# Kernel tuning notes

Hardware: AMD Instinct MI355X
Metric: run time of the kernel (lower is better)

## Reference

```python
import jax, jax.numpy as jnp
from jax import lax
import numpy as np

D_MODEL = 512
MODES = 16
B, S = 8, 4096
EPS = 1e-5


def setup_inputs() -> dict:
    key = jax.random.key(0)
    ks = jax.random.split(key, 7)
    x = jax.random.normal(ks[0], (B, S, D_MODEL), dtype=jnp.float32)
    gamma = jnp.ones((D_MODEL,), dtype=jnp.float32)
    beta = jnp.zeros((D_MODEL,), dtype=jnp.float32)
    # complex spectral weights stored as real/imag parts, torch init: randn(cfloat)*0.02
    wr = jax.random.normal(ks[1], (D_MODEL, MODES), dtype=jnp.float32) * 0.02
    wi = jax.random.normal(ks[2], (D_MODEL, MODES), dtype=jnp.float32) * 0.02
    # Conv1d(d_model, d_model, 3): weight (out, in, k), torch default uniform(-b, b)
    bound = 1.0 / np.sqrt(D_MODEL * 3)
    conv_w = jax.random.uniform(ks[3], (D_MODEL, D_MODEL, 3), dtype=jnp.float32, minval=-bound, maxval=bound)
    conv_b = jax.random.uniform(ks[4], (D_MODEL,), dtype=jnp.float32, minval=-bound, maxval=bound)
    return {"x": x, "gamma": gamma, "beta": beta, "wr": wr, "wi": wi,
            "conv_w": conv_w, "conv_b": conv_b}


def reference(x, gamma, beta, wr, wi, conv_w, conv_b):
    Bq, Sq, Dq = x.shape
    residual = x
    # LayerNorm over last dim (biased variance, eps=1e-5)
    mu = jnp.mean(x, axis=-1, keepdims=True)
    var = jnp.var(x, axis=-1, keepdims=True)
    xn = (x - mu) * lax.rsqrt(var + EPS) * gamma + beta
    # truncated-mode spectral conv: rfft along seq, multiply first `modes` bins, irfft
    xf = jnp.fft.rfft(xn, axis=1, norm='ortho')           # [B, S//2+1, D] complex
    m = min(wr.shape[1], xf.shape[1])
    w = (wr + 1j * wi).T[:m]                              # [m, D]
    out_ft = jnp.zeros_like(xf).at[:, :m, :].set(xf[:, :m, :] * w[None])
    xs = jnp.fft.irfft(out_ft, n=Sq, axis=1, norm='ortho')  # [B, S, D] real
    # Conv1d(k=3, pad=1) over seq dim on channel-first layout
    xc = lax.conv_general_dilated(
        xs.transpose(0, 2, 1), conv_w, window_strides=(1,), padding=[(1, 1)],
        dimension_numbers=('NCH', 'OIH', 'NCH'))
    xc = (xc + conv_b[None, :, None]).transpose(0, 2, 1)
    return residual + xs + xc
```

## Files before the change

kernel.cpp:

```cpp
#include <hip/hip_runtime.h>
#include <hip/hip_bf16.h>
#include <math.h>

#define Bn 8
#define Sn 4096
#define Dn 512
#define MODES 16
#define ANGF 0.0015339807878856412f

#define PART_OFF 0
#define Y_OFF 8388608
#define WTF_OFF 8519680
#define ZP_OFF 9306112
#define G_OFF 10878976
#define V_OFF 11010048
#define STATS_OFF 11018240

__global__ __launch_bounds__(256) void k_transpose_w(
    const float* __restrict__ cw, float* __restrict__ wTf) {
  int idx = blockIdx.x * 256 + threadIdx.x;
  int o = idx & 511;
  int d = (idx >> 9) & 511;
  int t = idx >> 18;
  wTf[idx] = cw[o * 1536 + d * 3 + t];
}

__global__ __launch_bounds__(256) void k_stats(const float* __restrict__ x,
                                               float2* __restrict__ stats) {
  int wave = threadIdx.x >> 6, lane = threadIdx.x & 63;
  int row0 = blockIdx.x * 32 + wave * 8;
  for (int j = 0; j < 8; ++j) {
    int row = row0 + j;
    const float4* px = (const float4*)(x + ((size_t)row << 9));
    float4 v0 = px[lane * 2];
    float4 v1 = px[lane * 2 + 1];
    float ps = v0.x + v0.y + v0.z + v0.w + v1.x + v1.y + v1.z + v1.w;
    float pq = v0.x * v0.x + v0.y * v0.y + v0.z * v0.z + v0.w * v0.w +
               v1.x * v1.x + v1.y * v1.y + v1.z * v1.z + v1.w * v1.w;
#pragma unroll
    for (int off = 32; off > 0; off >>= 1) {
      ps += __shfl_down(ps, off);
      pq += __shfl_down(pq, off);
    }
    if (lane == 0) {
      float mu = ps * (1.0f / Dn);
      float var = pq * (1.0f / Dn) - mu * mu;
      stats[row] = make_float2(mu, rsqrtf(var + 1e-5f));
    }
  }
}

__global__ __launch_bounds__(256) void k_project(
    const float* __restrict__ x, const float* __restrict__ gamma,
    const float* __restrict__ beta, const float2* __restrict__ stats,
    float* __restrict__ partials) {
  int blk = blockIdx.x;
  int b = blk >> 7;
  int c = (blk >> 1) & 63;
  int dh = blk & 1;
  int tid = threadIdx.x;
  int s_base = c * 64;
  int d = dh * 256 + tid;

  __shared__ float2 s_tw[64 * MODES];
  __shared__ float2 s_mv[64];
  if (tid < 64) s_mv[tid] = stats[(b << 12) + s_base + tid];
#pragma unroll
  for (int u = 0; u < 4; u++) {
    int e = tid * 4 + u;
    int r = e >> 4, k = e & 15;
    int m = ((s_base + r) * k) & (Sn - 1);
    float sn, cn;
    __sincosf((float)m * ANGF, &sn, &cn);
    s_tw[e] = make_float2(cn, sn);
  }
  __syncthreads();

  float g = gamma[d], be = beta[d];
  float accRe[MODES], accIm[MODES];
#pragma unroll
  for (int k = 0; k < MODES; k++) { accRe[k] = 0.f; accIm[k] = 0.f; }

  const float* xp = x + (((size_t)(b * Sn + s_base)) << 9) + d;
  float xv_n = xp[0];
  for (int r = 0; r < 64; ++r) {
    float xv = xv_n;
    if (r < 63) xv_n = xp[(size_t)(r + 1) << 9];
    float2 mv = s_mv[r];
    float xn = (xv - mv.x) * mv.y * g + be;
    const float2* tw = &s_tw[r * MODES];
#pragma unroll
    for (int k = 0; k < MODES; k++) {
      float2 cs = tw[k];
      accRe[k] += xn * cs.x;
      accIm[k] -= xn * cs.y;
    }
  }
  size_t base = ((size_t)(b * 64 + c)) * MODES;
  float2* P = (float2*)partials;
#pragma unroll
  for (int k = 0; k < MODES; k++)
    P[(base + k) * Dn + d] = make_float2(accRe[k], accIm[k]);
}

__global__ __launch_bounds__(256) void k_reduce_modes(
    const float* __restrict__ partials, const float* __restrict__ wr,
    const float* __restrict__ wi, float* __restrict__ Y) {
  int idx = blockIdx.x * 256 + threadIdx.x;
  int d = idx & 511;
  int k = (idx >> 9) & 15;
  int b = idx >> 13;
  const float2* P = (const float2*)partials;
  float re = 0.f, im = 0.f;
#pragma unroll 8
  for (int c = 0; c < 64; c++) {
    float2 p = P[(((size_t)(b * 64 + c)) * MODES + k) * Dn + d];
    re += p.x;
    im += p.y;
  }
  float wrv = wr[d * MODES + k];
  float wiv = wi[d * MODES + k];
  float yre = re * wrv - im * wiv;
  float yim = re * wiv + im * wrv;
  float scale = (k == 0) ? (1.0f / 4096.0f) : (2.0f / 4096.0f);
  ((float2*)Y)[((size_t)b * MODES + k) * Dn + d] =
      make_float2(yre * scale, yim * scale);
}

__global__ __launch_bounds__(256) void k_build_z(
    const float* __restrict__ Y, const float* __restrict__ wTf,
    float* __restrict__ Zp) {
  int blk = blockIdx.x;
  int b = blk / 96;
  int rem = blk % 96;
  int t = rem >> 5;
  int r2 = rem & 31;
  int och = r2 >> 2;
  int dch = r2 & 3;
  int tid = threadIdx.x;
  int oi = tid & 63, kq = tid >> 6;
  int o = och * 64 + oi;
  int d0 = dch * 128;

  __shared__ float2 Ys[MODES][128];
  const float2* Y2 = (const float2*)Y;
#pragma unroll
  for (int i = 0; i < 8; i++) {
    int e = tid + i * 256;
    int k = e >> 7, dd = e & 127;
    Ys[k][dd] = Y2[(((size_t)(b * MODES + k)) << 9) + d0 + dd];
  }
  __syncthreads();

  float zc[4] = {0.f, 0.f, 0.f, 0.f}, zs[4] = {0.f, 0.f, 0.f, 0.f};
  const float* wp = wTf + (((size_t)(t * Dn + d0)) << 9) + o;
  float wv_n = wp[0];
  for (int dd = 0; dd < 128; ++dd) {
    float wv = wv_n;
    if (dd < 127) wv_n = wp[(size_t)(dd + 1) << 9];
#pragma unroll
    for (int m = 0; m < 4; m++) {
      float2 y = Ys[kq * 4 + m][dd];
      zc[m] += y.x * wv;
      zs[m] += y.y * wv;
    }
  }
  float2* Z2 = (float2*)Zp;
#pragma unroll
  for (int m = 0; m < 4; m++) {
    int k = kq * 4 + m;
    Z2[(((size_t)(dch * 24 + b * 3 + t) * MODES + k)) << 9 | o] =
        make_float2(zc[m], zs[m]);
  }
}

__global__ __launch_bounds__(256) void k_build_g(
    const float* __restrict__ Y, const float* __restrict__ Zp,
    float* __restrict__ G, float* __restrict__ V) {
  int idx = blockIdx.x * 256 + threadIdx.x;
  const float2* Y2 = (const float2*)Y;
  const float2* Z2 = (const float2*)Zp;
  if (idx < 65536) {
    int o = idx & 511;
    int k = (idx >> 9) & 15;
    int b = idx >> 13;
    float2 z0 = make_float2(0.f, 0.f), z1 = z0, z2 = z0;
#pragma unroll
    for (int dch = 0; dch < 4; dch++) {
      float2 a0 = Z2[(((size_t)(dch * 24 + b * 3 + 0) * MODES + k)) << 9 | o];
      float2 a1 = Z2[(((size_t)(dch * 24 + b * 3 + 1) * MODES + k)) << 9 | o];
      float2 a2 = Z2[(((size_t)(dch * 24 + b * 3 + 2) * MODES + k)) << 9 | o];
      z0.x += a0.x; z0.y += a0.y;
      z1.x += a1.x; z1.y += a1.y;
      z2.x += a2.x; z2.y += a2.y;
    }
    float2 y = Y2[(((size_t)(b * MODES + k)) << 9) + o];
    float sf, cf;
    __sincosf((float)k * ANGF, &sf, &cf);
    float gc = y.x + (cf * z0.x + sf * z0.y) + z1.x + (cf * z2.x - sf * z2.y);
    float gs = y.y + (cf * z0.y - sf * z0.x) + z1.y + (cf * z2.y + sf * z2.x);
    G[(((size_t)(b * MODES + k) * 2 + 0)) << 9 | o] = gc;
    G[(((size_t)(b * MODES + k) * 2 + 1)) << 9 | o] = gs;
  } else if (idx < 65536 + 8192) {
    int j = idx - 65536;
    int o = j & 511;
    int comp = (j >> 9) & 1;
    int b = j >> 10;
    float v = 0.f;
#pragma unroll
    for (int k = 0; k < MODES; k++) {
      float2 z = make_float2(0.f, 0.f);
#pragma unroll
      for (int dch = 0; dch < 4; dch++) {
        float2 a = Z2[(((size_t)(dch * 24 + b * 3 + (comp ? 2 : 0)) * MODES +
                        k)) << 9 | o];
        z.x += a.x; z.y += a.y;
      }
      if (comp == 0) {
        float sf, cf;
        __sincosf((float)k * ANGF, &sf, &cf);
        v += cf * z.x + sf * z.y;
      } else {
        v += z.x;
      }
    }
    V[((size_t)(b * 2 + comp) << 9) + o] = v;
  }
}

__global__ __launch_bounds__(256) void k_apply(
    const float* __restrict__ x, const float* __restrict__ G,
    const float* __restrict__ V, const float* __restrict__ conv_b,
    float* __restrict__ out) {
  int b = blockIdx.x >> 7;
  int st = blockIdx.x & 127;
  int s0 = st * 32;
  int tid = threadIdx.x;
  int o0 = tid * 2;

  __shared__ float2 s_tw[32][MODES];
#pragma unroll
  for (int u = 0; u < 2; u++) {
    int e = tid * 2 + u;
    int r = e >> 4, k = e & 15;
    int m = ((s0 + r) * k) & (Sn - 1);
    float sn, cn;
    __sincosf((float)m * ANGF, &sn, &cn);
    s_tw[r][k] = make_float2(cn, sn);
  }

  float2 Gc[MODES], Gs[MODES];
  const float2* Gp = (const float2*)(G + ((size_t)b * MODES * 2 * Dn));
#pragma unroll
  for (int k = 0; k < MODES; k++) {
    Gc[k] = Gp[(k * 2 + 0) * 256 + tid];
    Gs[k] = Gp[(k * 2 + 1) * 256 + tid];
  }
  float2 cb2 = *(const float2*)&conv_b[o0];
  __syncthreads();

  const float* xp = x + (((size_t)(b * Sn + s0)) << 9) + o0;
  float* op = out + (((size_t)(b * Sn + s0)) << 9) + o0;
  float2 xn_ = *(const float2*)xp;
  for (int rr = 0; rr < 32; ++rr) {
    float2 x2 = xn_;
    if (rr < 31) xn_ = *(const float2*)(xp + ((size_t)(rr + 1) << 9));
    float ax = 0.f, ay = 0.f;
    const float2* twr = s_tw[rr];
#pragma unroll
    for (int k = 0; k < MODES; k++) {
      float2 cs = twr[k];
      ax += cs.x * Gc[k].x - cs.y * Gs[k].x;
      ay += cs.x * Gc[k].y - cs.y * Gs[k].y;
    }
    int s = s0 + rr;
    if (s == 0) {
      float2 v = *(const float2*)&V[((size_t)(b * 2 + 0) << 9) + o0];
      ax -= v.x; ay -= v.y;
    }
    if (s == Sn - 1) {
      float2 v = *(const float2*)&V[((size_t)(b * 2 + 1) << 9) + o0];
      ax -= v.x; ay -= v.y;
    }
    float2 o2 = make_float2(x2.x + cb2.x + ax, x2.y + cb2.y + ay);
    *(float2*)(op + ((size_t)rr << 9)) = o2;
  }
}

extern "C" void kernel_launch(void* const* d_in, const int* in_sizes, int n_in,
                              void* d_out, int out_size, void* d_ws,
                              size_t ws_size, hipStream_t stream) {
  const float* x = (const float*)d_in[0];
  const float* gamma = (const float*)d_in[1];
  const float* beta = (const float*)d_in[2];
  const float* wr = (const float*)d_in[3];
  const float* wi = (const float*)d_in[4];
  const float* conv_w = (const float*)d_in[5];
  const float* conv_b = (const float*)d_in[6];
  float* out = (float*)d_out;

  float* ws = (float*)d_ws;
  float* partials = ws + PART_OFF;
  float* Y = ws + Y_OFF;
  float* wTf = ws + WTF_OFF;
  float* Zp = ws + ZP_OFF;
  float* G = ws + G_OFF;
  float* V = ws + V_OFF;
  float2* stats = (float2*)(ws + STATS_OFF);

  hipLaunchKernelGGL(k_transpose_w, dim3(3072), dim3(256), 0, stream, conv_w,
                     wTf);
  hipLaunchKernelGGL(k_stats, dim3(1024), dim3(256), 0, stream, x, stats);
  hipLaunchKernelGGL(k_project, dim3(1024), dim3(256), 0, stream, x, gamma,
                     beta, stats, partials);
  hipLaunchKernelGGL(k_reduce_modes, dim3(256), dim3(256), 0, stream, partials,
                     wr, wi, Y);
  hipLaunchKernelGGL(k_build_z, dim3(768), dim3(256), 0, stream, Y, wTf, Zp);
  hipLaunchKernelGGL(k_build_g, dim3(288), dim3(256), 0, stream, Y, Zp, G, V);
  hipLaunchKernelGGL(k_apply, dim3(1024), dim3(256), 0, stream, x, G, V,
                     conv_b, out);
}
```

Baseline: 212.1 us.

## Exploit quarter-period twiddle symmetry in projection and apply kernels

Both the forward mode projection and the inverse apply kernel now process four sequence positions spaced S/4 apart together. Because the twiddle for mode k at those positions differs only by a power of i, a radix-4 butterfly lets one twiddle row serve four rows, cutting shared-memory twiddle traffic and sincos work. k_project also handles two channels per thread with float2/float4 accesses and launches half as many blocks. This increases register use through float2 accumulators and the 4-way row buffers, which may lower occupancy.

```diff
diff --git a/kernel.cpp b/kernel.cpp
--- a/kernel.cpp
+++ b/kernel.cpp
@@ -55,52 +55,99 @@
     const float* __restrict__ beta, const float2* __restrict__ stats,
     float* __restrict__ partials) {
   int blk = blockIdx.x;
-  int b = blk >> 7;
-  int c = (blk >> 1) & 63;
-  int dh = blk & 1;
+  int b = blk >> 6;
+  int c = blk & 63;
   int tid = threadIdx.x;
-  int s_base = c * 64;
-  int d = dh * 256 + tid;
-
-  __shared__ float2 s_tw[64 * MODES];
+  int d0 = tid << 1;
+  int s_base = c << 4;
+
+  __shared__ __attribute__((aligned(16))) float2 s_tw[16][MODES];
   __shared__ float2 s_mv[64];
-  if (tid < 64) s_mv[tid] = stats[(b << 12) + s_base + tid];
-#pragma unroll
-  for (int u = 0; u < 4; u++) {
-    int e = tid * 4 + u;
-    int r = e >> 4, k = e & 15;
+  {
+    int r = tid >> 4, k = tid & 15;
     int m = ((s_base + r) * k) & (Sn - 1);
     float sn, cn;
     __sincosf((float)m * ANGF, &sn, &cn);
-    s_tw[e] = make_float2(cn, sn);
+    s_tw[r][k] = make_float2(cn, sn);
+    if (tid < 64) {
+      s_mv[tid] = stats[(b << 12) + ((tid >> 4) << 10) + s_base + (tid & 15)];
+    }
   }
   __syncthreads();
 
-  float g = gamma[d], be = beta[d];
-  float accRe[MODES], accIm[MODES];
-#pragma unroll
-  for (int k = 0; k < MODES; k++) { accRe[k] = 0.f; accIm[k] = 0.f; }
-
-  const float* xp = x + (((size_t)(b * Sn + s_base)) << 9) + d;
-  float xv_n = xp[0];
-  for (int r = 0; r < 64; ++r) {
-    float xv = xv_n;
-    if (r < 63) xv_n = xp[(size_t)(r + 1) << 9];
-    float2 mv = s_mv[r];
-    float xn = (xv - mv.x) * mv.y * g + be;
-    const float2* tw = &s_tw[r * MODES];
-#pragma unroll
-    for (int k = 0; k < MODES; k++) {
-      float2 cs = tw[k];
-      accRe[k] += xn * cs.x;
-      accIm[k] -= xn * cs.y;
-    }
-  }
+  float2 g = *(const float2*)(gamma + d0);
+  float2 be = *(const float2*)(beta + d0);
+
+  float2 accRe[MODES], accIm[MODES];
+#pragma unroll
+  for (int k = 0; k < MODES; k++) {
+    accRe[k] = make_float2(0.f, 0.f);
+    accIm[k] = make_float2(0.f, 0.f);
+  }
+
+  const float* xb = x + (((size_t)b << 12) << 9) + d0;
+  float2 cur[4], nxt[4];
+#pragma unroll
+  for (int j = 0; j < 4; ++j)
+    cur[j] = *(const float2*)(xb + ((size_t)((j << 10) + s_base) << 9));
+
+#pragma unroll 2
+  for (int r = 0; r < 16; ++r) {
+    if (r < 15) {
+#pragma unroll
+      for (int j = 0; j < 4; ++j)
+        nxt[j] =
+            *(const float2*)(xb + ((size_t)((j << 10) + s_base + r + 1) << 9));
+    }
+    float2 xn[4];
+#pragma unroll
+    for (int j = 0; j < 4; ++j) {
+      float2 mv = s_mv[(j << 4) + r];
+      float ax = mv.y * g.x, ay = mv.y * g.y;
+      xn[j] = make_float2((cur[j].x - mv.x) * ax + be.x,
+                          (cur[j].y - mv.x) * ay + be.y);
+    }
+    float2 t02p = make_float2(xn[0].x + xn[2].x, xn[0].y + xn[2].y);
+    float2 t02m = make_float2(xn[0].x - xn[2].x, xn[0].y - xn[2].y);
+    float2 t13p = make_float2(xn[1].x + xn[3].x, xn[1].y + xn[3].y);
+    float2 t13m = make_float2(xn[1].x - xn[3].x, xn[1].y - xn[3].y);
+    float2 u0 = make_float2(t02p.x + t13p.x, t02p.y + t13p.y);
+    float2 u1 = make_float2(t02p.x - t13p.x, t02p.y - t13p.y);
+
+    const float4* twr = (const float4*)&s_tw[r][0];
+#pragma unroll
+    for (int kk = 0; kk < 8; ++kk) {
+      float4 t2 = twr[kk];
+      const int k0 = 2 * kk, k1 = 2 * kk + 1;
+      {
+        float2 u = ((k0 & 3) == 0) ? u0 : u1;
+        accRe[k0].x += u.x * t2.x;
+        accRe[k0].y += u.y * t2.x;
+        accIm[k0].x -= u.x * t2.y;
+        accIm[k0].y -= u.y * t2.y;
+      }
+      if ((k1 & 3) == 1) {
+        accRe[k1].x += t2.z * t02m.x - t2.w * t13m.x;
+        accRe[k1].y += t2.z * t02m.y - t2.w * t13m.y;
+        accIm[k1].x -= t2.z * t13m.x + t2.w * t02m.x;
+        accIm[k1].y -= t2.z * t13m.y + t2.w * t02m.y;
+      } else {
+        accRe[k1].x += t2.z * t02m.x + t2.w * t13m.x;
+        accRe[k1].y += t2.z * t02m.y + t2.w * t13m.y;
+        accIm[k1].x += t2.z * t13m.x - t2.w * t02m.x;
+        accIm[k1].y += t2.z * t13m.y - t2.w * t02m.y;
+      }
+    }
+#pragma unroll
+    for (int j = 0; j < 4; ++j) cur[j] = nxt[j];
+  }
+
   size_t base = ((size_t)(b * 64 + c)) * MODES;
-  float2* P = (float2*)partials;
+  float4* P4 = (float4*)partials;
 #pragma unroll
   for (int k = 0; k < MODES; k++)
-    P[(base + k) * Dn + d] = make_float2(accRe[k], accIm[k]);
+    P4[(base + k) * 256 + tid] =
+        make_float4(accRe[k].x, accIm[k].x, accRe[k].y, accIm[k].y);
 }
 
 __global__ __launch_bounds__(256) void k_reduce_modes(
@@ -233,20 +280,18 @@
     const float* __restrict__ V, const float* __restrict__ conv_b,
     float* __restrict__ out) {
   int b = blockIdx.x >> 7;
-  int st = blockIdx.x & 127;
-  int s0 = st * 32;
+  int rt = blockIdx.x & 127;
+  int r0 = rt << 3;
   int tid = threadIdx.x;
-  int o0 = tid * 2;
-
-  __shared__ float2 s_tw[32][MODES];
-#pragma unroll
-  for (int u = 0; u < 2; u++) {
-    int e = tid * 2 + u;
-    int r = e >> 4, k = e & 15;
-    int m = ((s0 + r) * k) & (Sn - 1);
+  int o0 = tid << 1;
+
+  __shared__ __attribute__((aligned(16))) float2 s_tw[8][MODES];
+  if (tid < 128) {
+    int rr = tid >> 4, k = tid & 15;
+    int m = ((r0 + rr) * k) & (Sn - 1);
     float sn, cn;
     __sincosf((float)m * ANGF, &sn, &cn);
-    s_tw[r][k] = make_float2(cn, sn);
+    s_tw[rr][k] = make_float2(cn, sn);
   }
 
   float2 Gc[MODES], Gs[MODES];
@@ -259,31 +304,74 @@
   float2 cb2 = *(const float2*)&conv_b[o0];
   __syncthreads();
 
-  const float* xp = x + (((size_t)(b * Sn + s0)) << 9) + o0;
-  float* op = out + (((size_t)(b * Sn + s0)) << 9) + o0;
-  float2 xn_ = *(const float2*)xp;
-  for (int rr = 0; rr < 32; ++rr) {
-    float2 x2 = xn_;
-    if (rr < 31) xn_ = *(const float2*)(xp + ((size_t)(rr + 1) << 9));
-    float ax = 0.f, ay = 0.f;
-    const float2* twr = s_tw[rr];
-#pragma unroll
-    for (int k = 0; k < MODES; k++) {
-      float2 cs = twr[k];
-      ax += cs.x * Gc[k].x - cs.y * Gs[k].x;
-      ay += cs.x * Gc[k].y - cs.y * Gs[k].y;
-    }
-    int s = s0 + rr;
-    if (s == 0) {
-      float2 v = *(const float2*)&V[((size_t)(b * 2 + 0) << 9) + o0];
-      ax -= v.x; ay -= v.y;
-    }
-    if (s == Sn - 1) {
-      float2 v = *(const float2*)&V[((size_t)(b * 2 + 1) << 9) + o0];
-      ax -= v.x; ay -= v.y;
-    }
-    float2 o2 = make_float2(x2.x + cb2.x + ax, x2.y + cb2.y + ay);
-    *(float2*)(op + ((size_t)rr << 9)) = o2;
+  const float* xb = x + (((size_t)b << 12) << 9) + o0;
+  float* ob = out + (((size_t)b << 12) << 9) + o0;
+
+  float2 cur[4], nxt[4];
+#pragma unroll
+  for (int j = 0; j < 4; ++j)
+    cur[j] = *(const float2*)(xb + ((size_t)((j << 10) + r0) << 9));
+
+#pragma unroll 2
+  for (int rr = 0; rr < 8; ++rr) {
+    if (rr < 7) {
+#pragma unroll
+      for (int j = 0; j < 4; ++j)
+        nxt[j] = *(const float2*)(xb + ((size_t)((j << 10) + r0 + rr + 1) << 9));
+    }
+    float2 a0 = make_float2(0.f, 0.f), a1 = a0, a2 = a0, a3 = a0;
+    const float4* twr = (const float4*)&s_tw[rr][0];
+#pragma unroll
+    for (int kk = 0; kk < 8; ++kk) {
+      float4 t2 = twr[kk];
+#define APPLY_K(kidx, cc, ss)                                          \
+  {                                                                    \
+    float2 Pre = make_float2(cc * Gc[kidx].x - ss * Gs[kidx].x,        \
+                             cc * Gc[kidx].y - ss * Gs[kidx].y);       \
+    float2 Pim = make_float2(cc * Gs[kidx].x + ss * Gc[kidx].x,        \
+                             cc * Gs[kidx].y + ss * Gc[kidx].y);       \
+    a0.x += Pre.x; a0.y += Pre.y;                                      \
+    if (((kidx) & 3) == 0) {                                           \
+      a1.x += Pre.x; a1.y += Pre.y;                                    \
+      a2.x += Pre.x; a2.y += Pre.y;                                    \
+      a3.x += Pre.x; a3.y += Pre.y;                                    \
+    } else if (((kidx) & 3) == 1) {                                    \
+      a1.x -= Pim.x; a1.y -= Pim.y;                                    \
+      a2.x -= Pre.x; a2.y -= Pre.y;                                    \
+      a3.x += Pim.x; a3.y += Pim.y;                                    \
+    } else if (((kidx) & 3) == 2) {                                    \
+      a1.x -= Pre.x; a1.y -= Pre.y;                                    \
+      a2.x += Pre.x; a2.y += Pre.y;                                    \
+      a3.x -= Pre.x; a3.y -= Pre.y;                                    \
+    } else {                                                           \
+      a1.x += Pim.x; a1.y += Pim.y;                                    \
+      a2.x -= Pre.x; a2.y -= Pre.y;                                    \
+      a3.x -= Pim.x; a3.y -= Pim.y;                                    \
+    }                                                                  \
+  }
+      APPLY_K(2 * kk, t2.x, t2.y);
+      APPLY_K(2 * kk + 1, t2.z, t2.w);
+#undef APPLY_K
+    }
+    int s_r = r0 + rr;
+#pragma unroll
+    for (int j = 0; j < 4; ++j) {
+      float2 aj = (j == 0) ? a0 : (j == 1) ? a1 : (j == 2) ? a2 : a3;
+      int s = s_r + (j << 10);
+      float2 o2 = make_float2(cur[j].x + cb2.x + aj.x,
+                              cur[j].y + cb2.y + aj.y);
+      if (s == 0) {
+        float2 v = *(const float2*)&V[((size_t)(b * 2 + 0) << 9) + o0];
+        o2.x -= v.x; o2.y -= v.y;
+      }
+      if (s == Sn - 1) {
+        float2 v = *(const float2*)&V[((size_t)(b * 2 + 1) << 9) + o0];
+        o2.x -= v.x; o2.y -= v.y;
+      }
+      *(float2*)(ob + ((size_t)s << 9)) = o2;
+    }
+#pragma unroll
+    for (int j = 0; j < 4; ++j) cur[j] = nxt[j];
   }
 }
 
@@ -311,7 +399,7 @@
   hipLaunchKernelGGL(k_transpose_w, dim3(3072), dim3(256), 0, stream, conv_w,
                      wTf);
   hipLaunchKernelGGL(k_stats, dim3(1024), dim3(256), 0, stream, x, stats);
-  hipLaunchKernelGGL(k_project, dim3(1024), dim3(256), 0, stream, x, gamma,
+  hipLaunchKernelGGL(k_project, dim3(512), dim3(256), 0, stream, x, gamma,
                      beta, stats, partials);
   hipLaunchKernelGGL(k_reduce_modes, dim3(256), dim3(256), 0, stream, partials,
                      wr, wi, Y);
```

Measured after the change: 190.2 us. -10.3%, faster.
